# Optimization experiments

Measured on AMD Instinct MI355X. Metric: run time of the kernel, lower is better.

Reference implementation:

```python
import jax, jax.numpy as jnp
import numpy as np

N_NODES = 100000
N_EDGES = 3200000
N_GRAPHS = 256
VOCAB = 1500


def gcn_conv(x, edge_index, W, b, n_nodes):
    # x: [N, Fin], edge_index: [2, E] (row=source, col=target)
    h = x @ W  # [N, Fout]
    loops = jnp.arange(n_nodes, dtype=edge_index.dtype)
    row = jnp.concatenate([edge_index[0], loops])
    col = jnp.concatenate([edge_index[1], loops])
    # symmetric normalization with self-loops (PyG GCNConv default)
    deg = jax.ops.segment_sum(jnp.ones_like(col, dtype=h.dtype), col,
                              num_segments=n_nodes)
    dinv = jnp.where(deg > 0, jax.lax.rsqrt(deg), 0.0)
    norm = dinv[row] * dinv[col]  # [E+N]
    msg = h[row] * norm[:, None]  # gather + scale
    out = jax.ops.segment_sum(msg, col, num_segments=n_nodes)  # scatter-add
    return out + b


def setup_inputs() -> dict:
    key = jax.random.key(0)
    k = jax.random.split(key, 8)
    x_ids = jax.random.randint(k[0], (N_NODES,), 0, VOCAB)
    edge_index = jax.random.randint(k[1], (2, N_EDGES), 0, N_NODES)
    batch = jnp.sort(jax.random.randint(k[2], (N_NODES,), 0, N_GRAPHS))
    emb_table = jax.random.normal(k[3], (VOCAB, 16), dtype=jnp.float32)
    W1 = jax.random.normal(k[4], (16, 32), dtype=jnp.float32) * (1.0 / np.sqrt(16))
    b1 = jnp.zeros((32,), dtype=jnp.float32)
    W2 = jax.random.normal(k[5], (32, 41), dtype=jnp.float32) * (1.0 / np.sqrt(32))
    b2 = jnp.zeros((41,), dtype=jnp.float32)
    return {"x_ids": x_ids, "edge_index": edge_index, "batch": batch,
            "emb_table": emb_table, "W1": W1, "b1": b1, "W2": W2, "b2": b2}


def reference(x_ids, edge_index, batch, emb_table, W1, b1, W2, b2):
    x = emb_table[x_ids]                      # embedding lookup [N,16]
    x = gcn_conv(x, edge_index, W1, b1, N_NODES)
    x = jax.nn.relu(x)                        # dropout is identity in eval
    x = gcn_conv(x, edge_index, W2, b2, N_NODES)
    # scatter_add pooling over graphs in batch
    return jax.ops.segment_sum(x, batch, num_segments=N_GRAPHS)  # [G,41]
```

## Files before the change

### kernel.cpp

```cpp
#include <hip/hip_runtime.h>


constexpr int EPB = 16384;
constexpr int BSH = 8;
constexpr int BKTN = 1 << BSH;
constexpr int CAP = 10240;

__device__ inline unsigned short f2bf(float x) {
  unsigned u = __float_as_uint(x);
  u += 0x7FFF + ((u >> 16) & 1);
  return (unsigned short)(u >> 16);
}
__device__ inline float bf2f(unsigned short h) {
  return __uint_as_float((unsigned)h << 16);
}
__device__ inline unsigned pk(float a, float b) {
  return (unsigned)f2bf(a) | ((unsigned)f2bf(b) << 16);
}
__device__ __forceinline__ void add8(float acc[8], uint4 v) {
  acc[0] += bf2f(v.x & 0xFFFF); acc[1] += bf2f(v.x >> 16);
  acc[2] += bf2f(v.y & 0xFFFF); acc[3] += bf2f(v.y >> 16);
  acc[4] += bf2f(v.z & 0xFFFF); acc[5] += bf2f(v.z >> 16);
  acc[6] += bf2f(v.w & 0xFFFF); acc[7] += bf2f(v.w >> 16);
}

__device__ __forceinline__ void gather8(const unsigned short* __restrict__ base,
                                        const int* list, int st, int dg,
                                        float acc[8]) {
  int j = 0;
  for (; j + 4 <= dg; j += 4) {
    int r0 = list[st + j], r1 = list[st + j + 1];
    int r2 = list[st + j + 2], r3 = list[st + j + 3];
    uint4 v0 = *(const uint4*)(base + (size_t)r0 * 16);
    uint4 v1 = *(const uint4*)(base + (size_t)r1 * 16);
    uint4 v2 = *(const uint4*)(base + (size_t)r2 * 16);
    uint4 v3 = *(const uint4*)(base + (size_t)r3 * 16);
    add8(acc, v0); add8(acc, v1); add8(acc, v2); add8(acc, v3);
  }
  for (; j < dg; ++j)
    add8(acc, *(const uint4*)(base + (size_t)list[st + j] * 16));
}

__device__ __forceinline__ int swz(int b, int nblkp) {
  return (b & 7) * (nblkp >> 3) + (b >> 3);
}

__global__ __launch_bounds__(1024) void k_hist(const int* __restrict__ col, int E,
                                               int nbkt, int nblkp,
                                               int* __restrict__ hist) {
  __shared__ int h[512];
  int tid = threadIdx.x;
  int blk = swz(blockIdx.x, nblkp);
  for (int i = tid; i < nbkt; i += 1024) h[i] = 0;
  __syncthreads();
  int e0 = blk * EPB, e1 = min(E, e0 + EPB);
  for (int e = e0 + tid; e < e1; e += 1024) atomicAdd(&h[col[e] >> BSH], 1);
  __syncthreads();
  for (int b = tid; b < nbkt; b += 1024) hist[b * nblkp + blk] = h[b];
}

__global__ __launch_bounds__(1024) void k_scan_a(const int* __restrict__ hist, int tot,
                                                 int* __restrict__ off,
                                                 int* __restrict__ bsums) {
  __shared__ int sd[1024];
  int tid = threadIdx.x;
  int i = blockIdx.x * 1024 + tid;
  int v = (i < tot) ? hist[i] : 0;
  sd[tid] = v;
  __syncthreads();
  for (int o = 1; o < 1024; o <<= 1) {
    int u = (tid >= o) ? sd[tid - o] : 0;
    __syncthreads();
    sd[tid] += u;
    __syncthreads();
  }
  if (i < tot) off[i] = sd[tid] - v;
  if (tid == 1023) bsums[blockIdx.x] = sd[tid];
}

__global__ __launch_bounds__(1024) void k_scan_c(int tot, int nblkp, int nbkt, int E,
                                                 int nscan,
                                                 const int* __restrict__ bsums,
                                                 int* __restrict__ off,
                                                 int* __restrict__ bucket_off) {
  __shared__ int sd[1024];
  int tid = threadIdx.x, b = blockIdx.x;
  sd[tid] = (tid < b && tid < nscan) ? bsums[tid] : 0;
  __syncthreads();
  for (int o = 512; o >= 1; o >>= 1) {
    if (tid < o) sd[tid] += sd[tid + o];
    __syncthreads();
  }
  int sbase = sd[0];
  int i = b * 1024 + tid;
  if (i < tot) {
    int v = off[i] + sbase;
    off[i] = v;
    if (i % nblkp == 0) bucket_off[i / nblkp] = v;
  }
  if (i == 0) bucket_off[nbkt] = E;
}

__global__ __launch_bounds__(1024) void k_scatter(const int* __restrict__ row,
                                                  const int* __restrict__ col, int E,
                                                  int nbkt, int nblkp,
                                                  const int* __restrict__ off,
                                                  int* __restrict__ staging) {
  __shared__ int sbuf[EPB];
  __shared__ int cnt[512], sc[512], cur[512];
  int tid = threadIdx.x;
  int lane = tid & 63, wv = tid >> 6;
  int blk = swz(blockIdx.x, nblkp);
  if (tid < 512) cnt[tid] = 0;
  __syncthreads();
  int e0 = blk * EPB, e1 = min(E, e0 + EPB);
  for (int e = e0 + tid; e < e1; e += 1024)
    atomicAdd(&cnt[col[e] >> BSH], 1);
  __syncthreads();
  if (tid < 512) sc[tid] = cnt[tid];
  __syncthreads();
  for (int o = 1; o < 512; o <<= 1) {
    int u = (tid < 512 && tid >= o) ? sc[tid - o] : 0;
    __syncthreads();
    if (tid < 512) sc[tid] += u;
    __syncthreads();
  }
  if (tid < 512) { int st = sc[tid] - cnt[tid]; sc[tid] = st; cur[tid] = st; }
  __syncthreads();
  for (int e = e0 + tid; e < e1; e += 1024) {
    int c = col[e];
    int b = c >> BSH;
    int pos = atomicAdd(&cur[b], 1);
    sbuf[pos] = (row[e] << BSH) | (c & (BKTN - 1));
  }
  __syncthreads();
  for (int b = wv; b < nbkt; b += 16) {
    int lbeg = sc[b], lcnt = cnt[b];
    int g = off[b * nblkp + blk];
    for (int j = lane; j < lcnt; j += 64)
      staging[g + j] = sbuf[lbeg + j];
  }
}

__global__ __launch_bounds__(BKTN) void k_degprep(const int* __restrict__ staging,
                                                  const int* __restrict__ bucket_off,
                                                  const int* __restrict__ x_ids,
                                                  const float* __restrict__ emb,
                                                  int N,
                                                  float* __restrict__ dinv,
                                                  unsigned short* __restrict__ ag1) {
  __shared__ int cnt[BKTN];
  int tid = threadIdx.x, b = blockIdx.x;
  int beg = bucket_off[b], end = bucket_off[b + 1];
  cnt[tid] = 0;
  __syncthreads();
  for (int i = beg + tid; i < end; i += BKTN)
    atomicAdd(&cnt[staging[i] & (BKTN - 1)], 1);
  __syncthreads();
  int node = (b << BSH) + tid;
  if (node >= N) return;
  float d = rsqrtf((float)(cnt[tid] + 1));
  dinv[node] = d;
  const float* er = emb + (size_t)x_ids[node] * 16;
  float4 e0 = *(const float4*)(er);
  float4 e1 = *(const float4*)(er + 4);
  float4 e2 = *(const float4*)(er + 8);
  float4 e3 = *(const float4*)(er + 12);
  uint4 o0, o1;
  o0.x = pk(e0.x * d, e0.y * d); o0.y = pk(e0.z * d, e0.w * d);
  o0.z = pk(e1.x * d, e1.y * d); o0.w = pk(e1.z * d, e1.w * d);
  o1.x = pk(e2.x * d, e2.y * d); o1.y = pk(e2.z * d, e2.w * d);
  o1.z = pk(e3.x * d, e3.y * d); o1.w = pk(e3.z * d, e3.w * d);
  *(uint4*)(ag1 + (size_t)node * 16) = o0;
  *(uint4*)(ag1 + (size_t)node * 16 + 8) = o1;
}

__global__ __launch_bounds__(512) void k_fuse1(const unsigned short* __restrict__ ag1,
                                               const int* __restrict__ staging,
                                               const int* __restrict__ bucket_off,
                                               const float* __restrict__ dinv,
                                               const float* __restrict__ W1,
                                               const float* __restrict__ b1, int N,
                                               unsigned short* __restrict__ y1g) {
  __shared__ int list[CAP];
  __shared__ int cnt[BKTN], sc[BKTN], lcur[BKTN];
  __shared__ float W[512];
  __shared__ float bb[32];
  int tid = threadIdx.x, b = blockIdx.x;
  W[tid] = W1[tid];
  if (tid < 32) bb[tid] = b1[tid];
  int nloc = tid >> 1, half = tid & 1;
  int node = (b << BSH) + nloc;
  float acc[8];
  if (node < N) {
    uint4 v = *(const uint4*)(ag1 + (size_t)node * 16 + half * 8);
    acc[0] = bf2f(v.x & 0xFFFF); acc[1] = bf2f(v.x >> 16);
    acc[2] = bf2f(v.y & 0xFFFF); acc[3] = bf2f(v.y >> 16);
    acc[4] = bf2f(v.z & 0xFFFF); acc[5] = bf2f(v.z >> 16);
    acc[6] = bf2f(v.w & 0xFFFF); acc[7] = bf2f(v.w >> 16);
  } else {
#pragma unroll
    for (int k = 0; k < 8; ++k) acc[k] = 0.f;
  }
  int beg = bucket_off[b], end = bucket_off[b + 1];
  for (int cbeg = beg; cbeg < end; cbeg += CAP) {
    int cend = min(end, cbeg + CAP);
    if (tid < BKTN) cnt[tid] = 0;
    __syncthreads();
    for (int i = cbeg + tid; i < cend; i += 512)
      atomicAdd(&cnt[staging[i] & (BKTN - 1)], 1);
    __syncthreads();
    if (tid < BKTN) sc[tid] = cnt[tid];
    __syncthreads();
    for (int o = 1; o < BKTN; o <<= 1) {
      int u = (tid < BKTN && tid >= o) ? sc[tid - o] : 0;
      __syncthreads();
      if (tid < BKTN) sc[tid] += u;
      __syncthreads();
    }
    if (tid < BKTN) {
      int st = sc[tid] - cnt[tid];
      sc[tid] = st;
      lcur[tid] = st;
    }
    __syncthreads();
    for (int i = cbeg + tid; i < cend; i += 512) {
      int p = staging[i];
      int pos = atomicAdd(&lcur[p & (BKTN - 1)], 1);
      list[pos] = p >> BSH;
    }
    __syncthreads();
    if (node < N) gather8(ag1 + half * 8, list, sc[nloc], cnt[nloc], acc);
    __syncthreads();
  }
  if (node >= N) return;
  float d = dinv[node];
  float sx[8], xo[8];
#pragma unroll
  for (int k = 0; k < 8; ++k) sx[k] = acc[k] * d;
#pragma unroll
  for (int k = 0; k < 8; ++k) xo[k] = __shfl_xor(sx[k], 1);
  float x[16];
  if (half == 0) {
#pragma unroll
    for (int k = 0; k < 8; ++k) { x[k] = sx[k]; x[8 + k] = xo[k]; }
  } else {
#pragma unroll
    for (int k = 0; k < 8; ++k) { x[k] = xo[k]; x[8 + k] = sx[k]; }
  }
  int j0 = half * 16;
  float a[16];
#pragma unroll
  for (int j = 0; j < 16; ++j) a[j] = bb[j0 + j];
#pragma unroll
  for (int k = 0; k < 16; ++k) {
    float xv = x[k];
#pragma unroll
    for (int j = 0; j < 16; ++j) a[j] += xv * W[k * 32 + j0 + j];
  }
#pragma unroll
  for (int j = 0; j < 16; ++j) a[j] = fmaxf(a[j], 0.f) * d;
  uint4 o0 = {pk(a[0], a[1]), pk(a[2], a[3]), pk(a[4], a[5]), pk(a[6], a[7])};
  uint4 o1 = {pk(a[8], a[9]), pk(a[10], a[11]), pk(a[12], a[13]), pk(a[14], a[15])};
  unsigned short* yp = y1g + (size_t)half * N * 16 + (size_t)node * 16;
  *(uint4*)(yp) = o0;
  *(uint4*)(yp + 8) = o1;
}

__global__ __launch_bounds__(512) void k_fuse2(const unsigned short* __restrict__ y1p,
                                               const int* __restrict__ staging,
                                               const int* __restrict__ bucket_off,
                                               const float* __restrict__ dinv,
                                               const int* __restrict__ batch, int N,
                                               int pofs, float* __restrict__ P) {
  __shared__ int list[CAP];
  __shared__ int cnt[BKTN], sc[BKTN], lcur[BKTN];
  __shared__ float pool[8 * 16];
  int tid = threadIdx.x, b = blockIdx.x;
  int nloc = tid >> 1, half = tid & 1;
  int node = (b << BSH) + nloc;
  float acc[8];
  if (node < N) {
    uint4 v = *(const uint4*)(y1p + (size_t)node * 16 + half * 8);
    acc[0] = bf2f(v.x & 0xFFFF); acc[1] = bf2f(v.x >> 16);
    acc[2] = bf2f(v.y & 0xFFFF); acc[3] = bf2f(v.y >> 16);
    acc[4] = bf2f(v.z & 0xFFFF); acc[5] = bf2f(v.z >> 16);
    acc[6] = bf2f(v.w & 0xFFFF); acc[7] = bf2f(v.w >> 16);
  } else {
#pragma unroll
    for (int k = 0; k < 8; ++k) acc[k] = 0.f;
  }
  int beg = bucket_off[b], end = bucket_off[b + 1];
  for (int cbeg = beg; cbeg < end; cbeg += CAP) {
    int cend = min(end, cbeg + CAP);
    if (tid < BKTN) cnt[tid] = 0;
    __syncthreads();
    for (int i = cbeg + tid; i < cend; i += 512)
      atomicAdd(&cnt[staging[i] & (BKTN - 1)], 1);
    __syncthreads();
    if (tid < BKTN) sc[tid] = cnt[tid];
    __syncthreads();
    for (int o = 1; o < BKTN; o <<= 1) {
      int u = (tid < BKTN && tid >= o) ? sc[tid - o] : 0;
      __syncthreads();
      if (tid < BKTN) sc[tid] += u;
      __syncthreads();
    }
    if (tid < BKTN) {
      int st = sc[tid] - cnt[tid];
      sc[tid] = st;
      lcur[tid] = st;
    }
    __syncthreads();
    for (int i = cbeg + tid; i < cend; i += 512) {
      int p = staging[i];
      int pos = atomicAdd(&lcur[p & (BKTN - 1)], 1);
      list[pos] = p >> BSH;
    }
    __syncthreads();
    if (node < N) gather8(y1p + half * 8, list, sc[nloc], cnt[nloc], acc);
    __syncthreads();
  }
  int myg = -1;
  if (node < N) {
    float d = dinv[node];
#pragma unroll
    for (int k = 0; k < 8; ++k) acc[k] *= d;
    myg = batch[node];
  }
  int g0 = batch[b << BSH];
  int g1 = batch[min((b << BSH) + BKTN - 1, N - 1)];
  for (int clo = g0; clo <= g1; clo += 8) {
    for (int j = tid; j < 8 * 16; j += 512) pool[j] = 0.f;
    __syncthreads();
    if (myg >= clo && myg < clo + 8) {
      float* pp = pool + (myg - clo) * 16 + half * 8;
#pragma unroll
      for (int k = 0; k < 8; ++k) atomicAdd(pp + k, acc[k]);
    }
    __syncthreads();
    int ng = min(8, g1 - clo + 1);
    for (int j = tid; j < ng * 16; j += 512)
      atomicAdd(&P[(size_t)(clo + (j >> 4)) * 32 + pofs + (j & 15)], pool[j]);
    __syncthreads();
  }
}

__global__ __launch_bounds__(64) void k_final(const float* __restrict__ P,
                                              const int* __restrict__ batch, int N,
                                              const float* __restrict__ W2,
                                              const float* __restrict__ b2,
                                              float* __restrict__ out) {
  __shared__ float pr[32];
  __shared__ int se[2];
  int g = blockIdx.x, tid = threadIdx.x;
  if (tid < 2) {
    int v = g + tid;
    int lo = 0, hi = N;
    while (lo < hi) {
      int mid = (lo + hi) >> 1;
      if (batch[mid] < v) lo = mid + 1; else hi = mid;
    }
    se[tid] = lo;
  }
  if (tid < 32) pr[tid] = P[(size_t)g * 32 + tid];
  __syncthreads();
  if (tid < 41) {
    float o = (float)(se[1] - se[0]) * b2[tid];
#pragma unroll
    for (int k = 0; k < 32; ++k) o += pr[k] * W2[k * 41 + tid];
    out[(size_t)g * 41 + tid] = o;
  }
}

extern "C" void kernel_launch(void* const* d_in, const int* in_sizes, int n_in,
                              void* d_out, int out_size, void* d_ws, size_t ws_size,
                              hipStream_t stream) {
  const int* x_ids = (const int*)d_in[0];
  const int* edge_index = (const int*)d_in[1];
  const int* batch = (const int*)d_in[2];
  const float* emb = (const float*)d_in[3];
  const float* W1 = (const float*)d_in[4];
  const float* b1 = (const float*)d_in[5];
  const float* W2 = (const float*)d_in[6];
  const float* b2 = (const float*)d_in[7];
  float* out = (float*)d_out;

  const int N = in_sizes[0];
  const int E = in_sizes[1] / 2;
  const int G = out_size / 41;
  const int* row = edge_index;
  const int* col = edge_index + E;

  const int nbkt = (N + BKTN - 1) >> BSH;
  int nblk = (E + EPB - 1) / EPB;
  const int nblkp = (nblk + 7) & ~7;
  const int tot = nbkt * nblkp;
  const int nscan = (tot + 1023) >> 10;

  char* ws = (char*)d_ws;
  size_t woff = 0;
  auto alloc = [&](size_t bytes) -> char* {
    char* p = ws + woff;
    woff += (bytes + 255) & ~(size_t)255;
    return p;
  };
  int* staging = (int*)alloc((size_t)E * 4);
  float* dinv = (float*)alloc((size_t)N * 4);
  unsigned short* ag1 = (unsigned short*)alloc((size_t)N * 16 * 2);
  unsigned short* y1g = (unsigned short*)alloc((size_t)N * 32 * 2);
  int* hist = (int*)alloc((size_t)tot * 4);
  int* off = (int*)alloc((size_t)tot * 4);
  int* bucket_off = (int*)alloc(((size_t)nbkt + 1) * 4);
  int* bsums = (int*)alloc((size_t)nscan * 4);
  float* P = (float*)alloc((size_t)G * 32 * 4);
  (void)ws_size; (void)n_in;

  hipMemsetAsync(P, 0, (size_t)G * 32 * 4, stream);

  k_hist<<<nblkp, 1024, 0, stream>>>(col, E, nbkt, nblkp, hist);
  k_scan_a<<<nscan, 1024, 0, stream>>>(hist, tot, off, bsums);
  k_scan_c<<<nscan, 1024, 0, stream>>>(tot, nblkp, nbkt, E, nscan, bsums, off, bucket_off);
  k_scatter<<<nblkp, 1024, 0, stream>>>(row, col, E, nbkt, nblkp, off, staging);
  k_degprep<<<nbkt, BKTN, 0, stream>>>(staging, bucket_off, x_ids, emb, N, dinv, ag1);
  k_fuse1<<<nbkt, 512, 0, stream>>>(ag1, staging, bucket_off, dinv, W1, b1, N, y1g);
  k_fuse2<<<nbkt, 512, 0, stream>>>(y1g, staging, bucket_off, dinv, batch, N, 0, P);
  k_fuse2<<<nbkt, 512, 0, stream>>>(y1g + (size_t)N * 16, staging, bucket_off, dinv,
                                    batch, N, 16, P);
  k_final<<<G, 64, 0, stream>>>(P, batch, N, W2, b2, out);
}
```

Measured before the change: 239.5 us.

## Build CSR once in prep kernel and reuse it in all aggregation passes

The degree-prep kernel now also does the per-bucket counting sort once, writing a CSR column pointer array and a sorted edge_row array. The three aggregation kernels then load their chunk of edge_row into shared memory and gather over each node's CSR range. Before, each of those kernels repeated the shared-memory histogram, scan and atomic placement itself. This removes repeated atomics and barriers but adds one extra E-sized write and read of edge_row, plus more work in the prep kernel.

```diff
diff --git a/kernel.cpp b/kernel.cpp
--- a/kernel.cpp
+++ b/kernel.cpp
@@ -142,48 +142,79 @@
   }
 }
 
-__global__ __launch_bounds__(BKTN) void k_degprep(const int* __restrict__ staging,
-                                                  const int* __restrict__ bucket_off,
-                                                  const int* __restrict__ x_ids,
-                                                  const float* __restrict__ emb,
-                                                  int N,
-                                                  float* __restrict__ dinv,
-                                                  unsigned short* __restrict__ ag1) {
-  __shared__ int cnt[BKTN];
+__global__ __launch_bounds__(512) void k_build(const int* __restrict__ staging,
+                                               const int* __restrict__ bucket_off,
+                                               const int* __restrict__ x_ids,
+                                               const float* __restrict__ emb,
+                                               int N, int E,
+                                               int* __restrict__ col_ptr,
+                                               float* __restrict__ dinv,
+                                               unsigned short* __restrict__ ag1,
+                                               int* __restrict__ edge_row) {
+  __shared__ int list[CAP];
+  __shared__ int cnt[BKTN], sc[BKTN], lcur[BKTN];
   int tid = threadIdx.x, b = blockIdx.x;
   int beg = bucket_off[b], end = bucket_off[b + 1];
-  cnt[tid] = 0;
-  __syncthreads();
-  for (int i = beg + tid; i < end; i += BKTN)
+  if (tid < BKTN) cnt[tid] = 0;
+  __syncthreads();
+  for (int i = beg + tid; i < end; i += 512)
     atomicAdd(&cnt[staging[i] & (BKTN - 1)], 1);
   __syncthreads();
-  int node = (b << BSH) + tid;
-  if (node >= N) return;
-  float d = rsqrtf((float)(cnt[tid] + 1));
-  dinv[node] = d;
-  const float* er = emb + (size_t)x_ids[node] * 16;
-  float4 e0 = *(const float4*)(er);
-  float4 e1 = *(const float4*)(er + 4);
-  float4 e2 = *(const float4*)(er + 8);
-  float4 e3 = *(const float4*)(er + 12);
-  uint4 o0, o1;
-  o0.x = pk(e0.x * d, e0.y * d); o0.y = pk(e0.z * d, e0.w * d);
-  o0.z = pk(e1.x * d, e1.y * d); o0.w = pk(e1.z * d, e1.w * d);
-  o1.x = pk(e2.x * d, e2.y * d); o1.y = pk(e2.z * d, e2.w * d);
-  o1.z = pk(e3.x * d, e3.y * d); o1.w = pk(e3.z * d, e3.w * d);
-  *(uint4*)(ag1 + (size_t)node * 16) = o0;
-  *(uint4*)(ag1 + (size_t)node * 16 + 8) = o1;
+  if (tid < BKTN) sc[tid] = cnt[tid];
+  __syncthreads();
+  for (int o = 1; o < BKTN; o <<= 1) {
+    int u = (tid < BKTN && tid >= o) ? sc[tid - o] : 0;
+    __syncthreads();
+    if (tid < BKTN) sc[tid] += u;
+    __syncthreads();
+  }
+  if (tid < BKTN) {
+    int excl = sc[tid] - cnt[tid];
+    sc[tid] = excl;
+    lcur[tid] = excl;
+    int node = (b << BSH) + tid;
+    if (node < N) col_ptr[node] = beg + excl;
+  }
+  if (b == 0 && tid == 0) col_ptr[N] = E;
+  __syncthreads();
+  bool fits = (end - beg) <= CAP;
+  if (fits) {
+    for (int i = beg + tid; i < end; i += 512) {
+      int p = staging[i];
+      list[atomicAdd(&lcur[p & (BKTN - 1)], 1)] = p >> BSH;
+    }
+    __syncthreads();
+    for (int i = beg + tid; i < end; i += 512)
+      edge_row[i] = list[i - beg];
+  } else {
+    for (int i = beg + tid; i < end; i += 512) {
+      int p = staging[i];
+      edge_row[beg + atomicAdd(&lcur[p & (BKTN - 1)], 1)] = p >> BSH;
+    }
+  }
+  int nloc = tid >> 1, half = tid & 1;
+  int node = (b << BSH) + nloc;
+  if (node < N) {
+    float d = rsqrtf((float)(cnt[nloc] + 1));
+    if (half == 0) dinv[node] = d;
+    const float* er = emb + (size_t)x_ids[node] * 16 + half * 8;
+    float4 e0 = *(const float4*)(er);
+    float4 e1 = *(const float4*)(er + 4);
+    uint4 o;
+    o.x = pk(e0.x * d, e0.y * d); o.y = pk(e0.z * d, e0.w * d);
+    o.z = pk(e1.x * d, e1.y * d); o.w = pk(e1.z * d, e1.w * d);
+    *(uint4*)(ag1 + (size_t)node * 16 + half * 8) = o;
+  }
 }
 
 __global__ __launch_bounds__(512) void k_fuse1(const unsigned short* __restrict__ ag1,
-                                               const int* __restrict__ staging,
-                                               const int* __restrict__ bucket_off,
+                                               const int* __restrict__ edge_row,
+                                               const int* __restrict__ col_ptr,
                                                const float* __restrict__ dinv,
                                                const float* __restrict__ W1,
                                                const float* __restrict__ b1, int N,
                                                unsigned short* __restrict__ y1g) {
   __shared__ int list[CAP];
-  __shared__ int cnt[BKTN], sc[BKTN], lcur[BKTN];
   __shared__ float W[512];
   __shared__ float bb[32];
   int tid = threadIdx.x, b = blockIdx.x;
@@ -191,8 +222,14 @@
   if (tid < 32) bb[tid] = b1[tid];
   int nloc = tid >> 1, half = tid & 1;
   int node = (b << BSH) + nloc;
+  bool valid = node < N;
+  int beg = col_ptr[b << BSH];
+  int end = col_ptr[min((b + 1) << BSH, N)];
+  int ms = 0, me = 0;
   float acc[8];
-  if (node < N) {
+  if (valid) {
+    ms = col_ptr[node];
+    me = col_ptr[node + 1];
     uint4 v = *(const uint4*)(ag1 + (size_t)node * 16 + half * 8);
     acc[0] = bf2f(v.x & 0xFFFF); acc[1] = bf2f(v.x >> 16);
     acc[2] = bf2f(v.y & 0xFFFF); acc[3] = bf2f(v.y >> 16);
@@ -202,38 +239,17 @@
 #pragma unroll
     for (int k = 0; k < 8; ++k) acc[k] = 0.f;
   }
-  int beg = bucket_off[b], end = bucket_off[b + 1];
   for (int cbeg = beg; cbeg < end; cbeg += CAP) {
     int cend = min(end, cbeg + CAP);
-    if (tid < BKTN) cnt[tid] = 0;
-    __syncthreads();
-    for (int i = cbeg + tid; i < cend; i += 512)
-      atomicAdd(&cnt[staging[i] & (BKTN - 1)], 1);
-    __syncthreads();
-    if (tid < BKTN) sc[tid] = cnt[tid];
-    __syncthreads();
-    for (int o = 1; o < BKTN; o <<= 1) {
-      int u = (tid < BKTN && tid >= o) ? sc[tid - o] : 0;
-      __syncthreads();
-      if (tid < BKTN) sc[tid] += u;
-      __syncthreads();
-    }
-    if (tid < BKTN) {
-      int st = sc[tid] - cnt[tid];
-      sc[tid] = st;
-      lcur[tid] = st;
-    }
-    __syncthreads();
-    for (int i = cbeg + tid; i < cend; i += 512) {
-      int p = staging[i];
-      int pos = atomicAdd(&lcur[p & (BKTN - 1)], 1);
-      list[pos] = p >> BSH;
-    }
-    __syncthreads();
-    if (node < N) gather8(ag1 + half * 8, list, sc[nloc], cnt[nloc], acc);
-    __syncthreads();
-  }
-  if (node >= N) return;
+    __syncthreads();
+    for (int i = cbeg + tid; i < cend; i += 512) list[i - cbeg] = edge_row[i];
+    __syncthreads();
+    if (valid) {
+      int st = max(ms, cbeg), en = min(me, cend);
+      if (en > st) gather8(ag1 + half * 8, list, st - cbeg, en - st, acc);
+    }
+  }
+  if (!valid) return;
   float d = dinv[node];
   float sx[8], xo[8];
 #pragma unroll
@@ -268,19 +284,24 @@
 }
 
 __global__ __launch_bounds__(512) void k_fuse2(const unsigned short* __restrict__ y1p,
-                                               const int* __restrict__ staging,
-                                               const int* __restrict__ bucket_off,
+                                               const int* __restrict__ edge_row,
+                                               const int* __restrict__ col_ptr,
                                                const float* __restrict__ dinv,
                                                const int* __restrict__ batch, int N,
                                                int pofs, float* __restrict__ P) {
   __shared__ int list[CAP];
-  __shared__ int cnt[BKTN], sc[BKTN], lcur[BKTN];
   __shared__ float pool[8 * 16];
   int tid = threadIdx.x, b = blockIdx.x;
   int nloc = tid >> 1, half = tid & 1;
   int node = (b << BSH) + nloc;
+  bool valid = node < N;
+  int beg = col_ptr[b << BSH];
+  int end = col_ptr[min((b + 1) << BSH, N)];
+  int ms = 0, me = 0;
   float acc[8];
-  if (node < N) {
+  if (valid) {
+    ms = col_ptr[node];
+    me = col_ptr[node + 1];
     uint4 v = *(const uint4*)(y1p + (size_t)node * 16 + half * 8);
     acc[0] = bf2f(v.x & 0xFFFF); acc[1] = bf2f(v.x >> 16);
     acc[2] = bf2f(v.y & 0xFFFF); acc[3] = bf2f(v.y >> 16);
@@ -290,39 +311,18 @@
 #pragma unroll
     for (int k = 0; k < 8; ++k) acc[k] = 0.f;
   }
-  int beg = bucket_off[b], end = bucket_off[b + 1];
   for (int cbeg = beg; cbeg < end; cbeg += CAP) {
     int cend = min(end, cbeg + CAP);
-    if (tid < BKTN) cnt[tid] = 0;
-    __syncthreads();
-    for (int i = cbeg + tid; i < cend; i += 512)
-      atomicAdd(&cnt[staging[i] & (BKTN - 1)], 1);
-    __syncthreads();
-    if (tid < BKTN) sc[tid] = cnt[tid];
-    __syncthreads();
-    for (int o = 1; o < BKTN; o <<= 1) {
-      int u = (tid < BKTN && tid >= o) ? sc[tid - o] : 0;
-      __syncthreads();
-      if (tid < BKTN) sc[tid] += u;
-      __syncthreads();
-    }
-    if (tid < BKTN) {
-      int st = sc[tid] - cnt[tid];
-      sc[tid] = st;
-      lcur[tid] = st;
-    }
-    __syncthreads();
-    for (int i = cbeg + tid; i < cend; i += 512) {
-      int p = staging[i];
-      int pos = atomicAdd(&lcur[p & (BKTN - 1)], 1);
-      list[pos] = p >> BSH;
-    }
-    __syncthreads();
-    if (node < N) gather8(y1p + half * 8, list, sc[nloc], cnt[nloc], acc);
-    __syncthreads();
+    __syncthreads();
+    for (int i = cbeg + tid; i < cend; i += 512) list[i - cbeg] = edge_row[i];
+    __syncthreads();
+    if (valid) {
+      int st = max(ms, cbeg), en = min(me, cend);
+      if (en > st) gather8(y1p + half * 8, list, st - cbeg, en - st, acc);
+    }
   }
   int myg = -1;
-  if (node < N) {
+  if (valid) {
     float d = dinv[node];
 #pragma unroll
     for (int k = 0; k < 8; ++k) acc[k] *= d;
@@ -406,6 +406,8 @@
     return p;
   };
   int* staging = (int*)alloc((size_t)E * 4);
+  int* edge_row = (int*)alloc((size_t)E * 4);
+  int* col_ptr = (int*)alloc(((size_t)N + 1) * 4);
   float* dinv = (float*)alloc((size_t)N * 4);
   unsigned short* ag1 = (unsigned short*)alloc((size_t)N * 16 * 2);
   unsigned short* y1g = (unsigned short*)alloc((size_t)N * 32 * 2);
@@ -422,10 +424,11 @@
   k_scan_a<<<nscan, 1024, 0, stream>>>(hist, tot, off, bsums);
   k_scan_c<<<nscan, 1024, 0, stream>>>(tot, nblkp, nbkt, E, nscan, bsums, off, bucket_off);
   k_scatter<<<nblkp, 1024, 0, stream>>>(row, col, E, nbkt, nblkp, off, staging);
-  k_degprep<<<nbkt, BKTN, 0, stream>>>(staging, bucket_off, x_ids, emb, N, dinv, ag1);
-  k_fuse1<<<nbkt, 512, 0, stream>>>(ag1, staging, bucket_off, dinv, W1, b1, N, y1g);
-  k_fuse2<<<nbkt, 512, 0, stream>>>(y1g, staging, bucket_off, dinv, batch, N, 0, P);
-  k_fuse2<<<nbkt, 512, 0, stream>>>(y1g + (size_t)N * 16, staging, bucket_off, dinv,
+  k_build<<<nbkt, 512, 0, stream>>>(staging, bucket_off, x_ids, emb, N, E,
+                                    col_ptr, dinv, ag1, edge_row);
+  k_fuse1<<<nbkt, 512, 0, stream>>>(ag1, edge_row, col_ptr, dinv, W1, b1, N, y1g);
+  k_fuse2<<<nbkt, 512, 0, stream>>>(y1g, edge_row, col_ptr, dinv, batch, N, 0, P);
+  k_fuse2<<<nbkt, 512, 0, stream>>>(y1g + (size_t)N * 16, edge_row, col_ptr, dinv,
                                     batch, N, 16, P);
   k_final<<<G, 64, 0, stream>>>(P, batch, N, W2, b2, out);
 }
```

Result: faster. 227.5 us, median of 2 (-5.0%).
